# Performance work log

Measured on AMD Instinct MI355X. Metric: run time of the kernel, lower is better.

The kernel has to match this reference:

```python
import jax, jax.numpy as jnp
import numpy as np

B, T, IN_DIM, H, C = 2048, 512, 28, 64, 10


def setup_inputs() -> dict:
    key = jax.random.key(0)
    ks = jax.random.split(key, 7)
    s = 1.0 / np.sqrt(H)  # PyTorch RNN init scale
    u = lambda k, shape: jax.random.uniform(k, shape, jnp.float32, -s, s)
    return {
        "x": jax.random.normal(ks[0], (B, 1, T, IN_DIM), jnp.float32),
        "W_ih": u(ks[1], (3 * H, IN_DIM)),  # gates ordered (r, z, n)
        "W_hh": u(ks[2], (3 * H, H)),
        "b_ih": u(ks[3], (3 * H,)),
        "b_hh": u(ks[4], (3 * H,)),
        "W_out": u(ks[5], (C, H)),
        "b_out": u(ks[6], (C,)),
    }


def reference(x, W_ih, W_hh, b_ih, b_hh, W_out, b_out):
    x = x[:, 0]  # squeeze(1) -> [B, T, IN]
    # Precompute all input-to-gate projections once: [B, T, 3H]
    xg = jnp.einsum("bti,gi->btg", x, W_ih) + b_ih

    def step(h, xg_t):
        gh = h @ W_hh.T + b_hh                      # [B, 3H]
        xr, xz, xn = jnp.split(xg_t, 3, axis=-1)
        hr, hz, hn = jnp.split(gh, 3, axis=-1)
        r = jax.nn.sigmoid(xr + hr)
        z = jax.nn.sigmoid(xz + hz)
        n = jnp.tanh(xn + r * hn)
        h_new = (1.0 - z) * n + z * h
        return h_new, None

    h0 = jnp.zeros((x.shape[0], H), x.dtype)
    hT, _ = jax.lax.scan(step, h0, jnp.swapaxes(xg, 0, 1))  # scan over time
    logits = hT @ W_out.T + b_out                            # [B, C]
    return jax.nn.softmax(logits, axis=-1)
```

## Files before the change

### kernel.cpp

```cpp
#include <hip/hip_runtime.h>

#define BB     2048
#define TT     512
#define INDIM  28
#define HH     64
#define NC     10
#define ROWS   16
#define NTHREADS 256
#define LDH    104

typedef __attribute__((ext_vector_type(8))) _Float16 f16x8;
typedef __attribute__((ext_vector_type(4))) _Float16 f16x4;
typedef __attribute__((ext_vector_type(4))) float     f32x4;

__device__ __forceinline__ float frcp(float v)  { return __builtin_amdgcn_rcpf(v); }
__device__ __forceinline__ float fsig(float v)  { return frcp(1.f + __expf(-v)); }
__device__ __forceinline__ float ftanh_(float v){ return fmaf(-2.f, frcp(1.f + __expf(2.f*v)), 1.f); }

#define MFMA(A_, B_, C_) __builtin_amdgcn_mfma_f32_16x16x32_f16((A_), (B_), (C_), 0, 0, 0)

__device__ __forceinline__ void lds_barrier() {
    asm volatile("s_waitcnt lgkmcnt(0)" ::: "memory");
    __builtin_amdgcn_s_barrier();
}

extern "C" __global__ __launch_bounds__(NTHREADS, 1)
void gru_mfma(const float* __restrict__ x,
              const float* __restrict__ W_ih,
              const float* __restrict__ W_hh,
              const float* __restrict__ b_ih,
              const float* __restrict__ b_hh,
              const float* __restrict__ W_out,
              const float* __restrict__ b_out,
              float* __restrict__ out)
{
    __shared__ __align__(16) _Float16 H_[2][16][LDH];
    __shared__ float hs_f[ROWS][HH];
    __shared__ float lg[ROWS][NC];

    const int tid = threadIdx.x;
    const int w   = tid >> 6;
    const int l   = tid & 63;
    const int c   = l & 15;
    const int hi  = l >> 4;
    const int hi8 = hi * 8;
    const int u   = w * 16 + c;
    const int u0  = w * 16 + 4 * hi;
    const int r0  = blockIdx.x * ROWS;

    f16x8 Bh[9];
    {
        const int GS[9][2] = {{0,0},{0,1},{0,2},{1,0},{1,1},{1,2},{2,0},{2,1},{3,2}};
        #pragma unroll
        for (int f = 0; f < 9; ++f) {
            const int g = GS[f][0], s = GS[f][1];
            #pragma unroll
            for (int j = 0; j < 8; ++j) {
                const int k = s * 32 + hi8 + j;
                float v = 0.f;
                if (g == 2)      { if (k < 64) v = W_hh[(size_t)(u + 128) * HH + k]; }
                else if (g == 3) { if (k >= 64 && k < 64 + INDIM) v = W_ih[(size_t)(u + 128) * INDIM + (k - 64)]; }
                else {
                    const int ru = u + 64 * g;
                    if (k < 64)              v = W_hh[(size_t)ru * HH + k];
                    else if (k < 64 + INDIM) v = W_ih[(size_t)ru * INDIM + (k - 64)];
                }
                Bh[f][j] = (_Float16)v;
            }
        }
    }
    f32x4 bv_r, bv_z, bv_nh, bv_nx;
    #pragma unroll
    for (int i = 0; i < 4; ++i) {
        bv_r[i]  = b_ih[u0 + i]       + b_hh[u0 + i];
        bv_z[i]  = b_ih[u0 + i + 64]  + b_hh[u0 + i + 64];
        bv_nh[i] = b_hh[u0 + i + 128];
        bv_nx[i] = b_ih[u0 + i + 128];
    }

    for (int i = tid; i < 2 * 16 * LDH; i += NTHREADS) ((_Float16*)H_)[i] = (_Float16)0.f;

    const float* xlane = x + (size_t)(r0 + c) * (size_t)TT * INDIM + hi8;
    const float4 zf4 = {0.f, 0.f, 0.f, 0.f};
    float4 xa[8], xb[8];
    #pragma unroll
    for (int k = 0; k < 8; ++k) {
        xa[k] = *(const float4*)(xlane + (size_t)k * INDIM);
        xb[k] = (hi < 3) ? *(const float4*)(xlane + (size_t)k * INDIM + 4) : zf4;
    }
    __syncthreads();

    float h[4] = {0.f, 0.f, 0.f, 0.f};
    int p = 0;

    for (int g = 0; g < TT / 8; ++g) {
        #pragma unroll
        for (int k = 0; k < 8; ++k) {
            const int t = 8 * g + k;

            f16x8 xf;
            {
                const float v[8] = {xa[k].x, xa[k].y, xa[k].z, xa[k].w,
                                    xb[k].x, xb[k].y, xb[k].z, xb[k].w};
                #pragma unroll
                for (int j = 0; j < 8; ++j) xf[j] = (_Float16)v[j];
            }
            const f16x8 bf0 = *(const f16x8*)&H_[p][c][hi8];
            const f16x8 bf1 = *(const f16x8*)&H_[p][c][32 + hi8];

            f32x4 a0 = MFMA(Bh[0], bf0, bv_r);
            f32x4 a1 = MFMA(Bh[3], bf0, bv_z);
            f32x4 a2 = MFMA(Bh[6], bf0, bv_nh);
            a0 = MFMA(Bh[1], bf1, a0);
            a1 = MFMA(Bh[4], bf1, a1);
            a2 = MFMA(Bh[7], bf1, a2);
            a0 = MFMA(Bh[2], xf, a0);
            a1 = MFMA(Bh[5], xf, a1);
            f32x4 a3 = MFMA(Bh[8], xf, bv_nx);

            f16x4 hv;
            #pragma unroll
            for (int i = 0; i < 4; ++i) {
                const float rg = fsig(a0[i]);
                const float zg = fsig(a1[i]);
                const float ng = ftanh_(fmaf(rg, a2[i], a3[i]));
                h[i] = fmaf(zg, h[i] - ng, ng);
                hv[i] = (_Float16)h[i];
            }
            *(f16x4*)&H_[p ^ 1][c][u0] = hv;

            if (t + 8 < TT) {
                xa[k] = *(const float4*)(xlane + (size_t)(t + 8) * INDIM);
                if (hi < 3) xb[k] = *(const float4*)(xlane + (size_t)(t + 8) * INDIM + 4);
            }
            lds_barrier();
            p ^= 1;
        }
    }

    #pragma unroll
    for (int i = 0; i < 4; ++i) hs_f[c][u0 + i] = h[i];
    __syncthreads();
    if (tid < ROWS * NC) {
        const int rr = tid / NC, cc = tid % NC;
        float s = b_out[cc];
        const float* wo = W_out + (size_t)cc * HH;
        #pragma unroll
        for (int j = 0; j < HH; ++j) s = fmaf(wo[j], hs_f[rr][j], s);
        lg[rr][cc] = s;
    }
    __syncthreads();
    if (tid < ROWS) {
        float mx = -1e30f;
        #pragma unroll
        for (int cc = 0; cc < NC; ++cc) mx = fmaxf(mx, lg[tid][cc]);
        float e[NC]; float ssum = 0.f;
        #pragma unroll
        for (int cc = 0; cc < NC; ++cc) { e[cc] = __expf(lg[tid][cc] - mx); ssum += e[cc]; }
        const float inv = 1.f / ssum;
        float* op = out + (size_t)(r0 + tid) * NC;
        #pragma unroll
        for (int cc = 0; cc < NC; ++cc) op[cc] = e[cc] * inv;
    }
}

extern "C" void kernel_launch(void* const* d_in, const int* in_sizes, int n_in,
                              void* d_out, int out_size, void* d_ws, size_t ws_size,
                              hipStream_t stream) {
    const float* x     = (const float*)d_in[0];
    const float* W_ih  = (const float*)d_in[1];
    const float* W_hh  = (const float*)d_in[2];
    const float* b_ih  = (const float*)d_in[3];
    const float* b_hh  = (const float*)d_in[4];
    const float* W_out = (const float*)d_in[5];
    const float* b_out = (const float*)d_in[6];
    (void)in_sizes; (void)n_in; (void)d_ws; (void)ws_size; (void)out_size;

    gru_mfma<<<BB / ROWS, NTHREADS, 0, stream>>>(x, W_ih, W_hh, b_ih, b_hh,
                                                 W_out, b_out, (float*)d_out);
}
```

Baseline: 199.3 us.

## Interleave two independent row tiles per block to hide recurrence latency

Each block now processes 32 batch rows as two interleaved 16-row GRU chains, with separate LDS hidden-state buffers and shared weight fragments. The goal is to hide MFMA and transcendental latency in the serial time loop with an independent chain's instructions. In exchange, the grid is halved to 64 blocks, leaving more compute units idle, and per-step instruction count and register use roughly double. Input rows are also converted to fp16 when prefetched instead of when used.

```diff
diff --git a/kernel.cpp b/kernel.cpp
--- a/kernel.cpp
+++ b/kernel.cpp
@@ -22,6 +22,16 @@
 __device__ __forceinline__ void lds_barrier() {
     asm volatile("s_waitcnt lgkmcnt(0)" ::: "memory");
     __builtin_amdgcn_s_barrier();
+}
+
+__device__ __forceinline__ f16x8 load_x8(const float* p, bool full) {
+    const float4 a = *(const float4*)p;
+    float4 b = {0.f, 0.f, 0.f, 0.f};
+    if (full) b = *(const float4*)(p + 4);
+    f16x8 r;
+    r[0] = (_Float16)a.x; r[1] = (_Float16)a.y; r[2] = (_Float16)a.z; r[3] = (_Float16)a.w;
+    r[4] = (_Float16)b.x; r[5] = (_Float16)b.y; r[6] = (_Float16)b.z; r[7] = (_Float16)b.w;
+    return r;
 }
 
 extern "C" __global__ __launch_bounds__(NTHREADS, 1)
@@ -34,9 +44,10 @@
               const float* __restrict__ b_out,
               float* __restrict__ out)
 {
-    __shared__ __align__(16) _Float16 H_[2][16][LDH];
-    __shared__ float hs_f[ROWS][HH];
-    __shared__ float lg[ROWS][NC];
+    __shared__ __align__(16) _Float16 HA_[2][16][LDH];
+    __shared__ __align__(16) _Float16 HB_[2][16][LDH];
+    __shared__ float hs_f[2 * ROWS][HH];
+    __shared__ float lg[2 * ROWS][NC];
 
     const int tid = threadIdx.x;
     const int w   = tid >> 6;
@@ -46,7 +57,7 @@
     const int hi8 = hi * 8;
     const int u   = w * 16 + c;
     const int u0  = w * 16 + 4 * hi;
-    const int r0  = blockIdx.x * ROWS;
+    const int r0  = blockIdx.x * (2 * ROWS);
 
     f16x8 Bh[9];
     {
@@ -78,19 +89,24 @@
         bv_nx[i] = b_ih[u0 + i + 128];
     }
 
-    for (int i = tid; i < 2 * 16 * LDH; i += NTHREADS) ((_Float16*)H_)[i] = (_Float16)0.f;
-
-    const float* xlane = x + (size_t)(r0 + c) * (size_t)TT * INDIM + hi8;
-    const float4 zf4 = {0.f, 0.f, 0.f, 0.f};
-    float4 xa[8], xb[8];
+    for (int i = tid; i < 2 * 16 * LDH; i += NTHREADS) {
+        ((_Float16*)HA_)[i] = (_Float16)0.f;
+        ((_Float16*)HB_)[i] = (_Float16)0.f;
+    }
+
+    const bool  xfull  = (hi < 3);
+    const float* xlaneA = x + (size_t)(r0 + c)        * (size_t)TT * INDIM + hi8;
+    const float* xlaneB = x + (size_t)(r0 + ROWS + c) * (size_t)TT * INDIM + hi8;
+    f16x8 rgA[8], rgB[8];
     #pragma unroll
     for (int k = 0; k < 8; ++k) {
-        xa[k] = *(const float4*)(xlane + (size_t)k * INDIM);
-        xb[k] = (hi < 3) ? *(const float4*)(xlane + (size_t)k * INDIM + 4) : zf4;
+        rgA[k] = load_x8(xlaneA + (size_t)k * INDIM, xfull);
+        rgB[k] = load_x8(xlaneB + (size_t)k * INDIM, xfull);
     }
     __syncthreads();
 
-    float h[4] = {0.f, 0.f, 0.f, 0.f};
+    float hA[4] = {0.f, 0.f, 0.f, 0.f};
+    float hB[4] = {0.f, 0.f, 0.f, 0.f};
     int p = 0;
 
     for (int g = 0; g < TT / 8; ++g) {
@@ -98,40 +114,57 @@
         for (int k = 0; k < 8; ++k) {
             const int t = 8 * g + k;
 
-            f16x8 xf;
-            {
-                const float v[8] = {xa[k].x, xa[k].y, xa[k].z, xa[k].w,
-                                    xb[k].x, xb[k].y, xb[k].z, xb[k].w};
-                #pragma unroll
-                for (int j = 0; j < 8; ++j) xf[j] = (_Float16)v[j];
-            }
-            const f16x8 bf0 = *(const f16x8*)&H_[p][c][hi8];
-            const f16x8 bf1 = *(const f16x8*)&H_[p][c][32 + hi8];
-
-            f32x4 a0 = MFMA(Bh[0], bf0, bv_r);
-            f32x4 a1 = MFMA(Bh[3], bf0, bv_z);
-            f32x4 a2 = MFMA(Bh[6], bf0, bv_nh);
-            a0 = MFMA(Bh[1], bf1, a0);
-            a1 = MFMA(Bh[4], bf1, a1);
-            a2 = MFMA(Bh[7], bf1, a2);
-            a0 = MFMA(Bh[2], xf, a0);
-            a1 = MFMA(Bh[5], xf, a1);
-            f32x4 a3 = MFMA(Bh[8], xf, bv_nx);
-
-            f16x4 hv;
+            const f16x8 bfA0 = *(const f16x8*)&HA_[p][c][hi8];
+            const f16x8 bfA1 = *(const f16x8*)&HA_[p][c][32 + hi8];
+            const f16x8 bfB0 = *(const f16x8*)&HB_[p][c][hi8];
+            const f16x8 bfB1 = *(const f16x8*)&HB_[p][c][32 + hi8];
+            const f16x8 xfA = rgA[k];
+            const f16x8 xfB = rgB[k];
+
+            f32x4 a0 = MFMA(Bh[0], bfA0, bv_r);
+            f32x4 a1 = MFMA(Bh[3], bfA0, bv_z);
+            f32x4 a2 = MFMA(Bh[6], bfA0, bv_nh);
+            f32x4 b0 = MFMA(Bh[0], bfB0, bv_r);
+            f32x4 b1 = MFMA(Bh[3], bfB0, bv_z);
+            f32x4 b2 = MFMA(Bh[6], bfB0, bv_nh);
+            a0 = MFMA(Bh[1], bfA1, a0);
+            a1 = MFMA(Bh[4], bfA1, a1);
+            a2 = MFMA(Bh[7], bfA1, a2);
+            b0 = MFMA(Bh[1], bfB1, b0);
+            b1 = MFMA(Bh[4], bfB1, b1);
+            b2 = MFMA(Bh[7], bfB1, b2);
+            a0 = MFMA(Bh[2], xfA, a0);
+            a1 = MFMA(Bh[5], xfA, a1);
+            f32x4 a3 = MFMA(Bh[8], xfA, bv_nx);
+            b0 = MFMA(Bh[2], xfB, b0);
+            b1 = MFMA(Bh[5], xfB, b1);
+            f32x4 b3 = MFMA(Bh[8], xfB, bv_nx);
+
+            f16x4 hvA;
             #pragma unroll
             for (int i = 0; i < 4; ++i) {
                 const float rg = fsig(a0[i]);
                 const float zg = fsig(a1[i]);
                 const float ng = ftanh_(fmaf(rg, a2[i], a3[i]));
-                h[i] = fmaf(zg, h[i] - ng, ng);
-                hv[i] = (_Float16)h[i];
-            }
-            *(f16x4*)&H_[p ^ 1][c][u0] = hv;
+                hA[i] = fmaf(zg, hA[i] - ng, ng);
+                hvA[i] = (_Float16)hA[i];
+            }
+            *(f16x4*)&HA_[p ^ 1][c][u0] = hvA;
+
+            f16x4 hvB;
+            #pragma unroll
+            for (int i = 0; i < 4; ++i) {
+                const float rg = fsig(b0[i]);
+                const float zg = fsig(b1[i]);
+                const float ng = ftanh_(fmaf(rg, b2[i], b3[i]));
+                hB[i] = fmaf(zg, hB[i] - ng, ng);
+                hvB[i] = (_Float16)hB[i];
+            }
+            *(f16x4*)&HB_[p ^ 1][c][u0] = hvB;
 
             if (t + 8 < TT) {
-                xa[k] = *(const float4*)(xlane + (size_t)(t + 8) * INDIM);
-                if (hi < 3) xb[k] = *(const float4*)(xlane + (size_t)(t + 8) * INDIM + 4);
+                rgA[k] = load_x8(xlaneA + (size_t)(t + 8) * INDIM, xfull);
+                rgB[k] = load_x8(xlaneB + (size_t)(t + 8) * INDIM, xfull);
             }
             lds_barrier();
             p ^= 1;
@@ -139,10 +172,13 @@
     }
 
     #pragma unroll
-    for (int i = 0; i < 4; ++i) hs_f[c][u0 + i] = h[i];
+    for (int i = 0; i < 4; ++i) {
+        hs_f[c][u0 + i]        = hA[i];
+        hs_f[ROWS + c][u0 + i] = hB[i];
+    }
     __syncthreads();
-    if (tid < ROWS * NC) {
-        const int rr = tid / NC, cc = tid % NC;
+    for (int e = tid; e < 2 * ROWS * NC; e += NTHREADS) {
+        const int rr = e / NC, cc = e % NC;
         float s = b_out[cc];
         const float* wo = W_out + (size_t)cc * HH;
         #pragma unroll
@@ -150,7 +186,7 @@
         lg[rr][cc] = s;
     }
     __syncthreads();
-    if (tid < ROWS) {
+    if (tid < 2 * ROWS) {
         float mx = -1e30f;
         #pragma unroll
         for (int cc = 0; cc < NC; ++cc) mx = fmaxf(mx, lg[tid][cc]);
@@ -176,6 +212,6 @@
     const float* b_out = (const float*)d_in[6];
     (void)in_sizes; (void)n_in; (void)d_ws; (void)ws_size; (void)out_size;
 
-    gru_mfma<<<BB / ROWS, NTHREADS, 0, stream>>>(x, W_ih, W_hh, b_ih, b_hh,
-                                                 W_out, b_out, (float*)d_out);
-}
+    gru_mfma<<<BB / (2 * ROWS), NTHREADS, 0, stream>>>(x, W_ih, W_hh, b_ih, b_hh,
+                                                       W_out, b_out, (float*)d_out);
+}
```

Result: slower. 706.5 us (+254.5%).
